# Kernel tuning notes

Hardware: AMD Instinct MI355X
Metric: run time of the kernel (lower is better)

Reference implementation:

```python
import jax, jax.numpy as jnp
import numpy as np

N = 8192
F_IN = 128
F_OUT = 128
NEG_SLOPE = 0.2


def setup_inputs() -> dict:
    key = jax.random.key(0)
    k_h, k_adj, k_W, k_a = jax.random.split(key, 4)
    h = jax.random.normal(k_h, (N, F_IN), dtype=jnp.float32)
    # binary adjacency mask as float (the module multiplies scores by adj)
    adj = (jax.random.uniform(k_adj, (N, N)) < 0.05).astype(jnp.float32)
    # nn.Linear(in, out, bias=False): weight shape [out, in]
    W = jax.random.normal(k_W, (F_OUT, F_IN), dtype=jnp.float32) / np.sqrt(F_IN)
    # nn.Linear(2*out, 1, bias=False): weight shape [1, 2*out]
    a = jax.random.normal(k_a, (1, 2 * F_OUT), dtype=jnp.float32) / np.sqrt(2 * F_OUT)
    return {"h": h, "adj": adj, "W": W, "a": a}


def reference(h, adj, W, a):
    # Wh: [N, F_out]
    Wh = h @ W.T
    f = Wh.shape[-1]
    # a([Wh_i ; Wh_j]) factored: e[i, j] = leaky_relu(Wh[i]@a1 + Wh[j]@a2)
    a1 = a[0, :f]  # [F_out]
    a2 = a[0, f:]  # [F_out]
    s_i = Wh @ a1  # [N]
    s_j = Wh @ a2  # [N]
    e = jax.nn.leaky_relu(s_i[:, None] + s_j[None, :], NEG_SLOPE)  # [N, N]
    # faithful to original: softmax over dim=1 of e * adj (multiplicative mask)
    attention = jax.nn.softmax(e * adj, axis=1)  # [N, N]
    return attention @ Wh  # [N, F_out]
```

## Files before the change

kernel.cpp:

```cpp
#include <hip/hip_runtime.h>

#define N_NODES 8192
#define FDIM 128
#define NEG_SLOPE 0.2f

typedef short short8 __attribute__((ext_vector_type(8)));
typedef float floatx16 __attribute__((ext_vector_type(16)));

__device__ inline unsigned fkey(float x) {
  unsigned b = __float_as_uint(x);
  return (b & 0x80000000u) ? ~b : (b | 0x80000000u);
}
__device__ inline float fkey_dec(unsigned kk) {
  unsigned bb = (kk & 0x80000000u) ? (kk ^ 0x80000000u) : ~kk;
  return __uint_as_float(bb);
}
__device__ inline unsigned short bf16_rn(float x) {
  unsigned u = __float_as_uint(x);
  u += 0x7fffu + ((u >> 16) & 1u);
  return (unsigned short)(u >> 16);
}

__global__ __launch_bounds__(256) void wh_fused_kernel(
    const float* __restrict__ h, const float* __restrict__ W,
    const float* __restrict__ a, float* __restrict__ s1g,
    float* __restrict__ Bj, float* __restrict__ Dj,
    unsigned* __restrict__ s2max_key,
    unsigned short* __restrict__ Bfh, unsigned short* __restrict__ Bfl) {
  __shared__ float Wt[FDIM * 129];
  __shared__ float rows[32 * 132];
  const int t = threadIdx.x;
  const int base = blockIdx.x * 32;
  for (int it = 0; it < 64; ++it) {
    int idx = t + 256 * it;
    int o = idx >> 7, k = idx & 127;
    Wt[k * 129 + o] = W[idx];
  }
  for (int it = 0; it < 16; ++it) {
    int idx = t + 256 * it;
    int r = idx >> 7, col = idx & 127;
    rows[r * 132 + col] = h[(size_t)base * FDIM + idx];
  }
  __syncthreads();
  const int c4 = (t & 31) * 4;
  const int g = t >> 5;
  float acc[4][4];
#pragma unroll
  for (int rr = 0; rr < 4; ++rr)
#pragma unroll
    for (int cc = 0; cc < 4; ++cc) acc[rr][cc] = 0.f;
  for (int k = 0; k < FDIM; ++k) {
    float4 wv = *(const float4*)&Wt[k * 129 + c4];
    float rv[4];
#pragma unroll
    for (int rr = 0; rr < 4; ++rr) rv[rr] = rows[(4 * g + rr) * 132 + k];
#pragma unroll
    for (int rr = 0; rr < 4; ++rr) {
      acc[rr][0] += rv[rr] * wv.x;
      acc[rr][1] += rv[rr] * wv.y;
      acc[rr][2] += rv[rr] * wv.z;
      acc[rr][3] += rv[rr] * wv.w;
    }
  }
  {
    float4 a1c = *(const float4*)&a[c4];
    float4 a2c = *(const float4*)&a[FDIM + c4];
    float p1[4], p2[4];
#pragma unroll
    for (int rr = 0; rr < 4; ++rr) {
      p1[rr] = acc[rr][0] * a1c.x + acc[rr][1] * a1c.y +
               acc[rr][2] * a1c.z + acc[rr][3] * a1c.w;
      p2[rr] = acc[rr][0] * a2c.x + acc[rr][1] * a2c.y +
               acc[rr][2] * a2c.z + acc[rr][3] * a2c.w;
    }
#pragma unroll
    for (int rr = 0; rr < 4; ++rr)
      for (int off = 16; off; off >>= 1) {
        p1[rr] += __shfl_down(p1[rr], off, 32);
        p2[rr] += __shfl_down(p2[rr], off, 32);
      }
    if ((t & 31) == 0) {
      unsigned kmax = 0;
#pragma unroll
      for (int rr = 0; rr < 4; ++rr) {
        int r = base + 4 * g + rr;
        s1g[r] = p1[rr];
        Bj[r] = __expf(p2[rr]);
        Dj[r] = __expf(NEG_SLOPE * p2[rr]);
        unsigned kk = fkey(p2[rr]);
        kmax = kk > kmax ? kk : kmax;
      }
      atomicMax(s2max_key, kmax);
    }
  }
  __syncthreads();
  unsigned short* hbuf = (unsigned short*)Wt;
  unsigned short* lbuf = hbuf + 4096;
#pragma unroll
  for (int rr = 0; rr < 4; ++rr)
#pragma unroll
    for (int cc = 0; cc < 4; ++cc) {
      float x = acc[rr][cc];
      unsigned short hb = bf16_rn(x);
      float hf = __uint_as_float(((unsigned)hb) << 16);
      unsigned short lb = bf16_rn(x - hf);
      int lr = 4 * g + rr;
      int n = c4 + cc;
      int idx = (((lr >> 4) * 4 + (n >> 5)) * 64 + ((lr >> 3) & 1) * 32 +
                 (n & 31)) * 8 + (lr & 7);
      hbuf[idx] = hb;
      lbuf[idx] = lb;
    }
  __syncthreads();
  {
    const unsigned* hsrc = (const unsigned*)hbuf;
    const unsigned* lsrc = (const unsigned*)lbuf;
    unsigned* hdst = (unsigned*)(Bfh + (size_t)base * FDIM);
    unsigned* ldst = (unsigned*)(Bfl + (size_t)base * FDIM);
    for (int q = t; q < 2048; q += 256) { hdst[q] = hsrc[q]; ldst[q] = lsrc[q]; }
  }
}

__global__ __launch_bounds__(256) void gat_mfma_kernel(
    const float* __restrict__ adj,
    const unsigned short* __restrict__ Bfh,
    const unsigned short* __restrict__ Bfl,
    const float* __restrict__ s1g, const float* __restrict__ Bj,
    const float* __restrict__ Dj, const unsigned* __restrict__ s2max_key,
    float* __restrict__ num, float* __restrict__ l_ws) {
  __shared__ float cred[4 * 32 * FDIM];
  const int t = threadIdx.x;
  const int lane = t & 63;
  const int wave = t >> 6;
  const int rowgrp = blockIdx.x >> 1;
  const int ksplit = blockIdx.x & 1;
  const int hh = lane >> 5;
  const int m0 = rowgrp * 32 + (lane & 31);
  const int kbase = ksplit * 4096 + wave * 1024;

  const float s1i = s1g[m0];
  float pmv = s1i + fkey_dec(*s2max_key);
  pmv = pmv > 0.f ? pmv : NEG_SLOPE * pmv;
  const float m = fmaxf(pmv, 0.f);
  const float Ai = __expf(s1i - m);
  const float Ci = __expf(NEG_SLOPE * s1i - m);
  const float Ti = __expf(-s1i);
  const float em = __expf(-m);

  const float* adj_lane = adj + (size_t)m0 * N_NODES + hh * 8;
  const float* bj_lane = Bj + hh * 8;
  const float* dj_lane = Dj + hh * 8;
  const short8* BH = (const short8*)Bfh;
  const short8* BL = (const short8*)Bfl;

  floatx16 acc0, acc1, acc2, acc3;
#pragma unroll
  for (int i = 0; i < 16; ++i) { acc0[i] = 0.f; acc1[i] = 0.f; acc2[i] = 0.f; acc3[i] = 0.f; }
  float rsum = 0.f;

#pragma unroll 2
  for (int k = kbase; k < kbase + 1024; k += 16) {
    float4 a0 = *(const float4*)(adj_lane + k);
    float4 a1 = *(const float4*)(adj_lane + k + 4);
    float4 b0 = *(const float4*)(bj_lane + k);
    float4 b1 = *(const float4*)(bj_lane + k + 4);
    float4 d0 = *(const float4*)(dj_lane + k);
    float4 d1 = *(const float4*)(dj_lane + k + 4);
    size_t fb = ((size_t)(k >> 4) * 4) * 64 + lane;
    short8 bh0 = BH[fb],       bl0 = BL[fb];
    short8 bh1 = BH[fb + 64],  bl1 = BL[fb + 64];
    short8 bh2 = BH[fb + 128], bl2 = BL[fb + 128];
    short8 bh3 = BH[fb + 192], bl3 = BL[fb + 192];

    float av[8] = {a0.x, a0.y, a0.z, a0.w, a1.x, a1.y, a1.z, a1.w};
    float bv[8] = {b0.x, b0.y, b0.z, b0.w, b1.x, b1.y, b1.z, b1.w};
    float dv[8] = {d0.x, d0.y, d0.z, d0.w, d1.x, d1.y, d1.z, d1.w};
    float pv[8];
#pragma unroll
    for (int e = 0; e < 8; ++e) {
      bool cpos = bv[e] > Ti;
      float p = (cpos ? Ai : Ci) * (cpos ? bv[e] : dv[e]);
      p = (av[e] != 0.f) ? p : em;
      pv[e] = p;
      rsum += p;
    }
    union { uint4 u; short8 s; } pk;
    pk.u.x = (unsigned)bf16_rn(pv[0]) | ((unsigned)bf16_rn(pv[1]) << 16);
    pk.u.y = (unsigned)bf16_rn(pv[2]) | ((unsigned)bf16_rn(pv[3]) << 16);
    pk.u.z = (unsigned)bf16_rn(pv[4]) | ((unsigned)bf16_rn(pv[5]) << 16);
    pk.u.w = (unsigned)bf16_rn(pv[6]) | ((unsigned)bf16_rn(pv[7]) << 16);
    short8 af = pk.s;

    acc0 = __builtin_amdgcn_mfma_f32_32x32x16_bf16(af, bh0, acc0, 0, 0, 0);
    acc0 = __builtin_amdgcn_mfma_f32_32x32x16_bf16(af, bl0, acc0, 0, 0, 0);
    acc1 = __builtin_amdgcn_mfma_f32_32x32x16_bf16(af, bh1, acc1, 0, 0, 0);
    acc1 = __builtin_amdgcn_mfma_f32_32x32x16_bf16(af, bl1, acc1, 0, 0, 0);
    acc2 = __builtin_amdgcn_mfma_f32_32x32x16_bf16(af, bh2, acc2, 0, 0, 0);
    acc2 = __builtin_amdgcn_mfma_f32_32x32x16_bf16(af, bl2, acc2, 0, 0, 0);
    acc3 = __builtin_amdgcn_mfma_f32_32x32x16_bf16(af, bh3, acc3, 0, 0, 0);
    acc3 = __builtin_amdgcn_mfma_f32_32x32x16_bf16(af, bl3, acc3, 0, 0, 0);
  }

  rsum += __shfl_xor(rsum, 32);
  if (lane < 32) atomicAdd(&l_ws[rowgrp * 32 + lane], rsum);

#pragma unroll
  for (int reg = 0; reg < 16; ++reg) {
    int r = (reg & 3) + 8 * (reg >> 2) + 4 * hh;
    int cbase = (wave * 32 + r) * FDIM + (lane & 31);
    cred[cbase]      = acc0[reg];
    cred[cbase + 32] = acc1[reg];
    cred[cbase + 64] = acc2[reg];
    cred[cbase + 96] = acc3[reg];
  }
  __syncthreads();
#pragma unroll
  for (int q = 0; q < 16; ++q) {
    int idx = q * 256 + t;
    int r = idx >> 7, c = idx & 127;
    float s = cred[r * FDIM + c] + cred[(32 + r) * FDIM + c] +
              cred[(64 + r) * FDIM + c] + cred[(96 + r) * FDIM + c];
    atomicAdd(&num[(size_t)(rowgrp * 32 + r) * FDIM + c], s);
  }
}

__global__ __launch_bounds__(256) void norm_kernel(
    const float* __restrict__ num, const float* __restrict__ l_ws,
    float* __restrict__ out) {
  int idx = blockIdx.x * 256 + threadIdx.x;
  float4 v = ((const float4*)num)[idx];
  float li = l_ws[idx >> 5];
  ((float4*)out)[idx] =
      make_float4(v.x / li, v.y / li, v.z / li, v.w / li);
}

extern "C" void kernel_launch(void* const* d_in, const int* in_sizes, int n_in,
                              void* d_out, int out_size, void* d_ws, size_t ws_size,
                              hipStream_t stream) {
  const float* h   = (const float*)d_in[0];
  const float* adj = (const float*)d_in[1];
  const float* W   = (const float*)d_in[2];
  const float* a   = (const float*)d_in[3];
  float* out = (float*)d_out;
  float* num = (float*)d_ws;
  float* l_ws = num + (size_t)N_NODES * FDIM;
  unsigned* key = (unsigned*)(l_ws + N_NODES);
  float* s1 = (float*)(key + 1);
  float* Bj = s1 + N_NODES;
  float* Dj = Bj + N_NODES;
  unsigned short* Bfh = (unsigned short*)(Dj + N_NODES);
  unsigned short* Bfl = Bfh + (size_t)N_NODES * FDIM;

  hipMemsetAsync(num, 0, ((size_t)N_NODES * FDIM + N_NODES + 1) * sizeof(float),
                 stream);
  hipLaunchKernelGGL(wh_fused_kernel, dim3(N_NODES / 32), dim3(256), 0, stream,
                     h, W, a, s1, Bj, Dj, key, Bfh, Bfl);
  hipLaunchKernelGGL(gat_mfma_kernel, dim3(512), dim3(256), 0, stream,
                     adj, Bfh, Bfl, s1, Bj, Dj, key, num, l_ws);
  hipLaunchKernelGGL(norm_kernel, dim3(N_NODES * FDIM / 4 / 256), dim3(256), 0,
                     stream, num, l_ws, out);
}
```

Before: 481.4 us.

## Compress adjacency to bitmasks in LDS and compute 64-row tiles per block

Each block now handles 64 rows and a quarter of the columns. It first streams its adjacency tile with coalesced loads and packs it into ballot bitmasks in shared memory. The main loop then computes two 32-row MFMA tiles per wave, so each load of the Bf B-fragments and the Bj/Dj values serves twice as many rows, which halves B-operand traffic per output row. Cross-wave reduction now uses LDS atomics into a 64x128 buffer, followed by global atomics. The cost is more registers (occupancy hinted at 2 blocks), a serial bitmask prologue, and more global atomics per block because of the 4-way K split.

```diff
diff --git a/kernel.cpp b/kernel.cpp
--- a/kernel.cpp
+++ b/kernel.cpp
@@ -6,6 +6,7 @@
 
 typedef short short8 __attribute__((ext_vector_type(8)));
 typedef float floatx16 __attribute__((ext_vector_type(16)));
+typedef unsigned long long u64;
 
 __device__ inline unsigned fkey(float x) {
   unsigned b = __float_as_uint(x);
@@ -121,106 +122,165 @@
   }
 }
 
-__global__ __launch_bounds__(256) void gat_mfma_kernel(
+__global__ __launch_bounds__(256, 2) void gat_mfma_kernel(
     const float* __restrict__ adj,
     const unsigned short* __restrict__ Bfh,
     const unsigned short* __restrict__ Bfl,
     const float* __restrict__ s1g, const float* __restrict__ Bj,
     const float* __restrict__ Dj, const unsigned* __restrict__ s2max_key,
     float* __restrict__ num, float* __restrict__ l_ws) {
-  __shared__ float cred[4 * 32 * FDIM];
+  __shared__ u64 bits_l[64 * 34];
+  __shared__ float cred[64 * FDIM];
   const int t = threadIdx.x;
   const int lane = t & 63;
   const int wave = t >> 6;
-  const int rowgrp = blockIdx.x >> 1;
-  const int ksplit = blockIdx.x & 1;
-  const int hh = lane >> 5;
-  const int m0 = rowgrp * 32 + (lane & 31);
-  const int kbase = ksplit * 4096 + wave * 1024;
-
-  const float s1i = s1g[m0];
-  float pmv = s1i + fkey_dec(*s2max_key);
-  pmv = pmv > 0.f ? pmv : NEG_SLOPE * pmv;
-  const float m = fmaxf(pmv, 0.f);
-  const float Ai = __expf(s1i - m);
-  const float Ci = __expf(NEG_SLOPE * s1i - m);
-  const float Ti = __expf(-s1i);
-  const float em = __expf(-m);
-
-  const float* adj_lane = adj + (size_t)m0 * N_NODES + hh * 8;
-  const float* bj_lane = Bj + hh * 8;
-  const float* dj_lane = Dj + hh * 8;
+  const int rowgrp = blockIdx.x >> 2;
+  const int ksplit = blockIdx.x & 3;
+  const int grow0 = rowgrp * 64;
+  const int blockK0 = ksplit * 2048;
+
+  {
+    const int rb = wave * 16;
+    for (int rl = 0; rl < 16; ++rl) {
+      const int r = rb + rl;
+      const float4* src =
+          (const float4*)(adj + (size_t)(grow0 + r) * N_NODES + blockK0);
+      float4 va[8];
+#pragma unroll
+      for (int sg = 0; sg < 8; ++sg) va[sg] = src[sg * 64 + lane];
+#pragma unroll
+      for (int sg = 0; sg < 8; ++sg) {
+        u64 b0 = __ballot(va[sg].x != 0.f);
+        u64 b1 = __ballot(va[sg].y != 0.f);
+        u64 b2 = __ballot(va[sg].z != 0.f);
+        u64 b3 = __ballot(va[sg].w != 0.f);
+        if (lane < 2) {
+          u64 lo = lane ? b2 : b0;
+          u64 hi = lane ? b3 : b1;
+          u64* dst = &bits_l[r * 34 + sg * 4 + lane * 2];
+          dst[0] = lo;
+          dst[1] = hi;
+        }
+      }
+    }
+  }
+  for (int q = t; q < 64 * FDIM; q += 256) cred[q] = 0.f;
+  __syncthreads();
+
+  const int lq = lane & 31, hh = lane >> 5;
+  const int gr0 = grow0 + lq, gr1 = gr0 + 32;
+  const float s2m = fkey_dec(*s2max_key);
+  const float s10 = s1g[gr0], s11 = s1g[gr1];
+  float pm0 = s10 + s2m; pm0 = pm0 > 0.f ? pm0 : NEG_SLOPE * pm0;
+  float pm1 = s11 + s2m; pm1 = pm1 > 0.f ? pm1 : NEG_SLOPE * pm1;
+  const float m0 = fmaxf(pm0, 0.f), m1 = fmaxf(pm1, 0.f);
+  const float em0 = __expf(-m0), em1 = __expf(-m1);
+  const float Ai0 = __expf(s10 - m0), Ai1 = __expf(s11 - m1);
+  const float Ci0 = __expf(NEG_SLOPE * s10 - m0), Ci1 = __expf(NEG_SLOPE * s11 - m1);
+  const float Ti0 = __expf(-s10), Ti1 = __expf(-s11);
+
   const short8* BH = (const short8*)Bfh;
   const short8* BL = (const short8*)Bfl;
-
-  floatx16 acc0, acc1, acc2, acc3;
-#pragma unroll
-  for (int i = 0; i < 16; ++i) { acc0[i] = 0.f; acc1[i] = 0.f; acc2[i] = 0.f; acc3[i] = 0.f; }
-  float rsum = 0.f;
-
+  floatx16 acc[2][4];
+#pragma unroll
+  for (int mt = 0; mt < 2; ++mt)
+#pragma unroll
+    for (int nt = 0; nt < 4; ++nt)
+#pragma unroll
+      for (int i = 0; i < 16; ++i) acc[mt][nt][i] = 0.f;
+  float rsum0 = 0.f, rsum1 = 0.f;
+
+  for (int s = 0; s < 2; ++s) {
+    const int sg = wave * 2 + s;
+    const u64* bp0 = &bits_l[lq * 34 + sg * 4];
+    const u64* bp1 = &bits_l[(lq + 32) * 34 + sg * 4];
+    longlong2 t0 = *(const longlong2*)bp0;
+    longlong2 t1 = *(const longlong2*)(bp0 + 2);
+    longlong2 t2 = *(const longlong2*)bp1;
+    longlong2 t3 = *(const longlong2*)(bp1 + 2);
+    u64 w0[4] = {(u64)t0.x, (u64)t0.y, (u64)t1.x, (u64)t1.y};
+    u64 w1[4] = {(u64)t2.x, (u64)t2.y, (u64)t3.x, (u64)t3.y};
 #pragma unroll 2
-  for (int k = kbase; k < kbase + 1024; k += 16) {
-    float4 a0 = *(const float4*)(adj_lane + k);
-    float4 a1 = *(const float4*)(adj_lane + k + 4);
-    float4 b0 = *(const float4*)(bj_lane + k);
-    float4 b1 = *(const float4*)(bj_lane + k + 4);
-    float4 d0 = *(const float4*)(dj_lane + k);
-    float4 d1 = *(const float4*)(dj_lane + k + 4);
-    size_t fb = ((size_t)(k >> 4) * 4) * 64 + lane;
-    short8 bh0 = BH[fb],       bl0 = BL[fb];
-    short8 bh1 = BH[fb + 64],  bl1 = BL[fb + 64];
-    short8 bh2 = BH[fb + 128], bl2 = BL[fb + 128];
-    short8 bh3 = BH[fb + 192], bl3 = BL[fb + 192];
-
-    float av[8] = {a0.x, a0.y, a0.z, a0.w, a1.x, a1.y, a1.z, a1.w};
-    float bv[8] = {b0.x, b0.y, b0.z, b0.w, b1.x, b1.y, b1.z, b1.w};
-    float dv[8] = {d0.x, d0.y, d0.z, d0.w, d1.x, d1.y, d1.z, d1.w};
-    float pv[8];
-#pragma unroll
-    for (int e = 0; e < 8; ++e) {
-      bool cpos = bv[e] > Ti;
-      float p = (cpos ? Ai : Ci) * (cpos ? bv[e] : dv[e]);
-      p = (av[e] != 0.f) ? p : em;
-      pv[e] = p;
-      rsum += p;
-    }
-    union { uint4 u; short8 s; } pk;
-    pk.u.x = (unsigned)bf16_rn(pv[0]) | ((unsigned)bf16_rn(pv[1]) << 16);
-    pk.u.y = (unsigned)bf16_rn(pv[2]) | ((unsigned)bf16_rn(pv[3]) << 16);
-    pk.u.z = (unsigned)bf16_rn(pv[4]) | ((unsigned)bf16_rn(pv[5]) << 16);
-    pk.u.w = (unsigned)bf16_rn(pv[6]) | ((unsigned)bf16_rn(pv[7]) << 16);
-    short8 af = pk.s;
-
-    acc0 = __builtin_amdgcn_mfma_f32_32x32x16_bf16(af, bh0, acc0, 0, 0, 0);
-    acc0 = __builtin_amdgcn_mfma_f32_32x32x16_bf16(af, bl0, acc0, 0, 0, 0);
-    acc1 = __builtin_amdgcn_mfma_f32_32x32x16_bf16(af, bh1, acc1, 0, 0, 0);
-    acc1 = __builtin_amdgcn_mfma_f32_32x32x16_bf16(af, bl1, acc1, 0, 0, 0);
-    acc2 = __builtin_amdgcn_mfma_f32_32x32x16_bf16(af, bh2, acc2, 0, 0, 0);
-    acc2 = __builtin_amdgcn_mfma_f32_32x32x16_bf16(af, bl2, acc2, 0, 0, 0);
-    acc3 = __builtin_amdgcn_mfma_f32_32x32x16_bf16(af, bh3, acc3, 0, 0, 0);
-    acc3 = __builtin_amdgcn_mfma_f32_32x32x16_bf16(af, bl3, acc3, 0, 0, 0);
-  }
-
-  rsum += __shfl_xor(rsum, 32);
-  if (lane < 32) atomicAdd(&l_ws[rowgrp * 32 + lane], rsum);
+    for (int it = 0; it < 16; ++it) {
+      const int kg = blockK0 + sg * 256 + it * 16;
+      const int j8 = kg + hh * 8;
+      float4 b0 = *(const float4*)(Bj + j8);
+      float4 b1 = *(const float4*)(Bj + j8 + 4);
+      float4 d0 = *(const float4*)(Dj + j8);
+      float4 d1 = *(const float4*)(Dj + j8 + 4);
+      size_t fb = ((size_t)(kg >> 4)) * 256 + lane;
+      short8 xh0 = BH[fb],       xl0 = BL[fb];
+      short8 xh1 = BH[fb + 64],  xl1 = BL[fb + 64];
+      short8 xh2 = BH[fb + 128], xl2 = BL[fb + 128];
+      short8 xh3 = BH[fb + 192], xl3 = BL[fb + 192];
+      float bvv[8] = {b0.x, b0.y, b0.z, b0.w, b1.x, b1.y, b1.z, b1.w};
+      float dvv[8] = {d0.x, d0.y, d0.z, d0.w, d1.x, d1.y, d1.z, d1.w};
+      const int bsh = it * 4 + hh * 2;
+      float pv0[8], pv1[8];
+#pragma unroll
+      for (int e = 0; e < 8; ++e) {
+        const int sh = bsh + (e >> 2);
+        float f0 = (float)((unsigned)(w0[e & 3] >> sh) & 1u);
+        float f1 = (float)((unsigned)(w1[e & 3] >> sh) & 1u);
+        bool cp0 = bvv[e] > Ti0, cp1 = bvv[e] > Ti1;
+        float q0 = (cp0 ? Ai0 : Ci0) * (cp0 ? bvv[e] : dvv[e]);
+        float q1 = (cp1 ? Ai1 : Ci1) * (cp1 ? bvv[e] : dvv[e]);
+        float p0 = em0 + f0 * (q0 - em0);
+        float p1 = em1 + f1 * (q1 - em1);
+        rsum0 += p0; rsum1 += p1;
+        pv0[e] = p0; pv1[e] = p1;
+      }
+      union { uint4 u; short8 s8; } k0, k1;
+      k0.u.x = (unsigned)bf16_rn(pv0[0]) | ((unsigned)bf16_rn(pv0[1]) << 16);
+      k0.u.y = (unsigned)bf16_rn(pv0[2]) | ((unsigned)bf16_rn(pv0[3]) << 16);
+      k0.u.z = (unsigned)bf16_rn(pv0[4]) | ((unsigned)bf16_rn(pv0[5]) << 16);
+      k0.u.w = (unsigned)bf16_rn(pv0[6]) | ((unsigned)bf16_rn(pv0[7]) << 16);
+      k1.u.x = (unsigned)bf16_rn(pv1[0]) | ((unsigned)bf16_rn(pv1[1]) << 16);
+      k1.u.y = (unsigned)bf16_rn(pv1[2]) | ((unsigned)bf16_rn(pv1[3]) << 16);
+      k1.u.z = (unsigned)bf16_rn(pv1[4]) | ((unsigned)bf16_rn(pv1[5]) << 16);
+      k1.u.w = (unsigned)bf16_rn(pv1[6]) | ((unsigned)bf16_rn(pv1[7]) << 16);
+      short8 af0 = k0.s8, af1 = k1.s8;
+      acc[0][0] = __builtin_amdgcn_mfma_f32_32x32x16_bf16(af0, xh0, acc[0][0], 0, 0, 0);
+      acc[0][0] = __builtin_amdgcn_mfma_f32_32x32x16_bf16(af0, xl0, acc[0][0], 0, 0, 0);
+      acc[0][1] = __builtin_amdgcn_mfma_f32_32x32x16_bf16(af0, xh1, acc[0][1], 0, 0, 0);
+      acc[0][1] = __builtin_amdgcn_mfma_f32_32x32x16_bf16(af0, xl1, acc[0][1], 0, 0, 0);
+      acc[0][2] = __builtin_amdgcn_mfma_f32_32x32x16_bf16(af0, xh2, acc[0][2], 0, 0, 0);
+      acc[0][2] = __builtin_amdgcn_mfma_f32_32x32x16_bf16(af0, xl2, acc[0][2], 0, 0, 0);
+      acc[0][3] = __builtin_amdgcn_mfma_f32_32x32x16_bf16(af0, xh3, acc[0][3], 0, 0, 0);
+      acc[0][3] = __builtin_amdgcn_mfma_f32_32x32x16_bf16(af0, xl3, acc[0][3], 0, 0, 0);
+      acc[1][0] = __builtin_amdgcn_mfma_f32_32x32x16_bf16(af1, xh0, acc[1][0], 0, 0, 0);
+      acc[1][0] = __builtin_amdgcn_mfma_f32_32x32x16_bf16(af1, xl0, acc[1][0], 0, 0, 0);
+      acc[1][1] = __builtin_amdgcn_mfma_f32_32x32x16_bf16(af1, xh1, acc[1][1], 0, 0, 0);
+      acc[1][1] = __builtin_amdgcn_mfma_f32_32x32x16_bf16(af1, xl1, acc[1][1], 0, 0, 0);
+      acc[1][2] = __builtin_amdgcn_mfma_f32_32x32x16_bf16(af1, xh2, acc[1][2], 0, 0, 0);
+      acc[1][2] = __builtin_amdgcn_mfma_f32_32x32x16_bf16(af1, xl2, acc[1][2], 0, 0, 0);
+      acc[1][3] = __builtin_amdgcn_mfma_f32_32x32x16_bf16(af1, xh3, acc[1][3], 0, 0, 0);
+      acc[1][3] = __builtin_amdgcn_mfma_f32_32x32x16_bf16(af1, xl3, acc[1][3], 0, 0, 0);
+    }
+  }
+
+  rsum0 += __shfl_xor(rsum0, 32);
+  rsum1 += __shfl_xor(rsum1, 32);
+  if (lane < 32) {
+    atomicAdd(&l_ws[gr0], rsum0);
+    atomicAdd(&l_ws[gr1], rsum1);
+  }
 
 #pragma unroll
   for (int reg = 0; reg < 16; ++reg) {
-    int r = (reg & 3) + 8 * (reg >> 2) + 4 * hh;
-    int cbase = (wave * 32 + r) * FDIM + (lane & 31);
-    cred[cbase]      = acc0[reg];
-    cred[cbase + 32] = acc1[reg];
-    cred[cbase + 64] = acc2[reg];
-    cred[cbase + 96] = acc3[reg];
-  }
-  __syncthreads();
-#pragma unroll
-  for (int q = 0; q < 16; ++q) {
-    int idx = q * 256 + t;
-    int r = idx >> 7, c = idx & 127;
-    float s = cred[r * FDIM + c] + cred[(32 + r) * FDIM + c] +
-              cred[(64 + r) * FDIM + c] + cred[(96 + r) * FDIM + c];
-    atomicAdd(&num[(size_t)(rowgrp * 32 + r) * FDIM + c], s);
+    const int r = (reg & 3) + 8 * (reg >> 2) + 4 * hh;
+#pragma unroll
+    for (int nt = 0; nt < 4; ++nt) {
+      atomicAdd(&cred[r * FDIM + nt * 32 + lq], acc[0][nt][reg]);
+      atomicAdd(&cred[(r + 32) * FDIM + nt * 32 + lq], acc[1][nt][reg]);
+    }
+  }
+  __syncthreads();
+#pragma unroll
+  for (int q = 0; q < 32; ++q) {
+    const int idx = q * 256 + t;
+    atomicAdd(&num[(size_t)(grow0 + (idx >> 7)) * FDIM + (idx & 127)],
+              cred[idx]);
   }
 }
 
@@ -230,8 +290,7 @@
   int idx = blockIdx.x * 256 + threadIdx.x;
   float4 v = ((const float4*)num)[idx];
   float li = l_ws[idx >> 5];
-  ((float4*)out)[idx] =
-      make_float4(v.x / li, v.y / li, v.z / li, v.w / li);
+  ((float4*)out)[idx] = make_float4(v.x / li, v.y / li, v.z / li, v.w / li);
 }
 
 extern "C" void kernel_launch(void* const* d_in, const int* in_sizes, int n_in,
```

Result: slower. 539.9 us (+12.1%).

## Factor out masked-entry constant, drop bf16 low split, pack adjacency as ballot bitmasks

Applied to the files above, without the earlier changes.

Masked entries all carry the same value exp(-m), so their contribution is handled analytically: the kernel accumulates (p - em) only on nonzero adj entries, and the norm pass adds em times a column sum S of Wh plus N*em to the denominator. The bf16 hi/lo split of Wh is dropped, which halves the B-operand loads and MFMA count but lowers precision. Adjacency is read with coalesced row-wise float4 loads, turned into ballot bitmasks in LDS, and the K range is split four ways across 1024 blocks. Partial results are reduced with LDS atomics into a single 32x128 buffer before the global atomics.

```diff
diff --git a/kernel.cpp b/kernel.cpp
--- a/kernel.cpp
+++ b/kernel.cpp
@@ -6,16 +6,17 @@
 
 typedef short short8 __attribute__((ext_vector_type(8)));
 typedef float floatx16 __attribute__((ext_vector_type(16)));
-
-__device__ inline unsigned fkey(float x) {
+typedef unsigned long long u64;
+
+static __device__ inline unsigned fkey(float x) {
   unsigned b = __float_as_uint(x);
   return (b & 0x80000000u) ? ~b : (b | 0x80000000u);
 }
-__device__ inline float fkey_dec(unsigned kk) {
+static __device__ inline float fkey_dec(unsigned kk) {
   unsigned bb = (kk & 0x80000000u) ? (kk ^ 0x80000000u) : ~kk;
   return __uint_as_float(bb);
 }
-__device__ inline unsigned short bf16_rn(float x) {
+static __device__ inline unsigned short bf16_rn(float x) {
   unsigned u = __float_as_uint(x);
   u += 0x7fffu + ((u >> 16) & 1u);
   return (unsigned short)(u >> 16);
@@ -24,9 +25,8 @@
 __global__ __launch_bounds__(256) void wh_fused_kernel(
     const float* __restrict__ h, const float* __restrict__ W,
     const float* __restrict__ a, float* __restrict__ s1g,
-    float* __restrict__ Bj, float* __restrict__ Dj,
-    unsigned* __restrict__ s2max_key,
-    unsigned short* __restrict__ Bfh, unsigned short* __restrict__ Bfl) {
+    float* __restrict__ Bj, float* __restrict__ Dj, float* __restrict__ S,
+    unsigned* __restrict__ s2max_key, unsigned short* __restrict__ WHf) {
   __shared__ float Wt[FDIM * 129];
   __shared__ float rows[32 * 132];
   const int t = threadIdx.x;
@@ -95,143 +95,170 @@
   }
   __syncthreads();
   unsigned short* hbuf = (unsigned short*)Wt;
-  unsigned short* lbuf = hbuf + 4096;
 #pragma unroll
   for (int rr = 0; rr < 4; ++rr)
 #pragma unroll
     for (int cc = 0; cc < 4; ++cc) {
-      float x = acc[rr][cc];
-      unsigned short hb = bf16_rn(x);
-      float hf = __uint_as_float(((unsigned)hb) << 16);
-      unsigned short lb = bf16_rn(x - hf);
       int lr = 4 * g + rr;
       int n = c4 + cc;
       int idx = (((lr >> 4) * 4 + (n >> 5)) * 64 + ((lr >> 3) & 1) * 32 +
                  (n & 31)) * 8 + (lr & 7);
-      hbuf[idx] = hb;
-      lbuf[idx] = lb;
-    }
+      hbuf[idx] = bf16_rn(acc[rr][cc]);
+    }
+  float4 cs = make_float4(acc[0][0] + acc[1][0] + acc[2][0] + acc[3][0],
+                          acc[0][1] + acc[1][1] + acc[2][1] + acc[3][1],
+                          acc[0][2] + acc[1][2] + acc[2][2] + acc[3][2],
+                          acc[0][3] + acc[1][3] + acc[2][3] + acc[3][3]);
+  *(float4*)&rows[g * FDIM + c4] = cs;
   __syncthreads();
   {
     const unsigned* hsrc = (const unsigned*)hbuf;
-    const unsigned* lsrc = (const unsigned*)lbuf;
-    unsigned* hdst = (unsigned*)(Bfh + (size_t)base * FDIM);
-    unsigned* ldst = (unsigned*)(Bfl + (size_t)base * FDIM);
-    for (int q = t; q < 2048; q += 256) { hdst[q] = hsrc[q]; ldst[q] = lsrc[q]; }
+    unsigned* hdst = (unsigned*)(WHf + (size_t)base * FDIM);
+    for (int q = t; q < 2048; q += 256) hdst[q] = hsrc[q];
+  }
+  if (t < FDIM) {
+    float s = 0.f;
+#pragma unroll
+    for (int gg = 0; gg < 8; ++gg) s += rows[gg * FDIM + t];
+    atomicAdd(&S[t], s);
   }
 }
 
 __global__ __launch_bounds__(256) void gat_mfma_kernel(
-    const float* __restrict__ adj,
-    const unsigned short* __restrict__ Bfh,
-    const unsigned short* __restrict__ Bfl,
+    const float* __restrict__ adj, const unsigned short* __restrict__ WHf,
     const float* __restrict__ s1g, const float* __restrict__ Bj,
     const float* __restrict__ Dj, const unsigned* __restrict__ s2max_key,
     float* __restrict__ num, float* __restrict__ l_ws) {
-  __shared__ float cred[4 * 32 * FDIM];
+  __shared__ u64 bits[4][32][4];
+  __shared__ float cred[32 * FDIM];
   const int t = threadIdx.x;
   const int lane = t & 63;
   const int wave = t >> 6;
-  const int rowgrp = blockIdx.x >> 1;
-  const int ksplit = blockIdx.x & 1;
-  const int hh = lane >> 5;
-  const int m0 = rowgrp * 32 + (lane & 31);
-  const int kbase = ksplit * 4096 + wave * 1024;
-
-  const float s1i = s1g[m0];
-  float pmv = s1i + fkey_dec(*s2max_key);
-  pmv = pmv > 0.f ? pmv : NEG_SLOPE * pmv;
-  const float m = fmaxf(pmv, 0.f);
-  const float Ai = __expf(s1i - m);
-  const float Ci = __expf(NEG_SLOPE * s1i - m);
-  const float Ti = __expf(-s1i);
-  const float em = __expf(-m);
-
-  const float* adj_lane = adj + (size_t)m0 * N_NODES + hh * 8;
-  const float* bj_lane = Bj + hh * 8;
-  const float* dj_lane = Dj + hh * 8;
-  const short8* BH = (const short8*)Bfh;
-  const short8* BL = (const short8*)Bfl;
-
-  floatx16 acc0, acc1, acc2, acc3;
-#pragma unroll
-  for (int i = 0; i < 16; ++i) { acc0[i] = 0.f; acc1[i] = 0.f; acc2[i] = 0.f; acc3[i] = 0.f; }
-  float rsum = 0.f;
-
+  const int lq = lane & 31, hh = lane >> 5;
+  const int rowgrp = blockIdx.x >> 2;
+  const int ksplit = blockIdx.x & 3;
+  const int grow = rowgrp * 32;
+  const int kw0 = ksplit * 2048 + wave * 512;
+
+  for (int q = t; q < 32 * FDIM; q += 256) cred[q] = 0.f;
+  __syncthreads();
+
+  const float s2m = fkey_dec(*s2max_key);
+  const float s1r = s1g[grow + lq];
+  float pm = s1r + s2m;
+  pm = pm > 0.f ? pm : NEG_SLOPE * pm;
+  const float mr = fmaxf(pm, 0.f);
+  const float emr = __expf(-mr);
+  const float Ar = __expf(s1r - mr);
+  const float Cr = __expf(NEG_SLOPE * s1r - mr);
+  const float Tr = __expf(-s1r);
+
+  const short8* BW = (const short8*)WHf;
+  floatx16 acc[4];
+#pragma unroll
+  for (int nt = 0; nt < 4; ++nt)
+#pragma unroll
+    for (int i = 0; i < 16; ++i) acc[nt][i] = 0.f;
+  float lv = 0.f;
+  u64* mybits = &bits[wave][0][0];
+
+  for (int s = 0; s < 2; ++s) {
+    const int c0 = kw0 + s * 256;
+    const float4* ap = (const float4*)(adj + (size_t)grow * N_NODES + c0);
 #pragma unroll 2
-  for (int k = kbase; k < kbase + 1024; k += 16) {
-    float4 a0 = *(const float4*)(adj_lane + k);
-    float4 a1 = *(const float4*)(adj_lane + k + 4);
-    float4 b0 = *(const float4*)(bj_lane + k);
-    float4 b1 = *(const float4*)(bj_lane + k + 4);
-    float4 d0 = *(const float4*)(dj_lane + k);
-    float4 d1 = *(const float4*)(dj_lane + k + 4);
-    size_t fb = ((size_t)(k >> 4) * 4) * 64 + lane;
-    short8 bh0 = BH[fb],       bl0 = BL[fb];
-    short8 bh1 = BH[fb + 64],  bl1 = BL[fb + 64];
-    short8 bh2 = BH[fb + 128], bl2 = BL[fb + 128];
-    short8 bh3 = BH[fb + 192], bl3 = BL[fb + 192];
-
-    float av[8] = {a0.x, a0.y, a0.z, a0.w, a1.x, a1.y, a1.z, a1.w};
-    float bv[8] = {b0.x, b0.y, b0.z, b0.w, b1.x, b1.y, b1.z, b1.w};
-    float dv[8] = {d0.x, d0.y, d0.z, d0.w, d1.x, d1.y, d1.z, d1.w};
-    float pv[8];
-#pragma unroll
-    for (int e = 0; e < 8; ++e) {
-      bool cpos = bv[e] > Ti;
-      float p = (cpos ? Ai : Ci) * (cpos ? bv[e] : dv[e]);
-      p = (av[e] != 0.f) ? p : em;
-      pv[e] = p;
-      rsum += p;
-    }
-    union { uint4 u; short8 s; } pk;
-    pk.u.x = (unsigned)bf16_rn(pv[0]) | ((unsigned)bf16_rn(pv[1]) << 16);
-    pk.u.y = (unsigned)bf16_rn(pv[2]) | ((unsigned)bf16_rn(pv[3]) << 16);
-    pk.u.z = (unsigned)bf16_rn(pv[4]) | ((unsigned)bf16_rn(pv[5]) << 16);
-    pk.u.w = (unsigned)bf16_rn(pv[6]) | ((unsigned)bf16_rn(pv[7]) << 16);
-    short8 af = pk.s;
-
-    acc0 = __builtin_amdgcn_mfma_f32_32x32x16_bf16(af, bh0, acc0, 0, 0, 0);
-    acc0 = __builtin_amdgcn_mfma_f32_32x32x16_bf16(af, bl0, acc0, 0, 0, 0);
-    acc1 = __builtin_amdgcn_mfma_f32_32x32x16_bf16(af, bh1, acc1, 0, 0, 0);
-    acc1 = __builtin_amdgcn_mfma_f32_32x32x16_bf16(af, bl1, acc1, 0, 0, 0);
-    acc2 = __builtin_amdgcn_mfma_f32_32x32x16_bf16(af, bh2, acc2, 0, 0, 0);
-    acc2 = __builtin_amdgcn_mfma_f32_32x32x16_bf16(af, bl2, acc2, 0, 0, 0);
-    acc3 = __builtin_amdgcn_mfma_f32_32x32x16_bf16(af, bh3, acc3, 0, 0, 0);
-    acc3 = __builtin_amdgcn_mfma_f32_32x32x16_bf16(af, bl3, acc3, 0, 0, 0);
-  }
-
-  rsum += __shfl_xor(rsum, 32);
-  if (lane < 32) atomicAdd(&l_ws[rowgrp * 32 + lane], rsum);
-
+    for (int rb = 0; rb < 32; rb += 8) {
+      float4 va[8];
+#pragma unroll
+      for (int r = 0; r < 8; ++r)
+        va[r] = ap[(size_t)(rb + r) * (N_NODES / 4) + lane];
+#pragma unroll
+      for (int r = 0; r < 8; ++r) {
+        u64 b0 = __ballot(va[r].x != 0.f);
+        u64 b1 = __ballot(va[r].y != 0.f);
+        u64 b2 = __ballot(va[r].z != 0.f);
+        u64 b3 = __ballot(va[r].w != 0.f);
+        if (lane == 0) {
+          u64* d = &mybits[(rb + r) * 4];
+          d[0] = b0; d[1] = b1; d[2] = b2; d[3] = b3;
+        }
+      }
+    }
+    ulonglong2 q0 = *(const ulonglong2*)&mybits[lq * 4];
+    ulonglong2 q1 = *(const ulonglong2*)&mybits[lq * 4 + 2];
+    const u64 ws0 = q0.x, ws1 = q0.y, ws2 = q1.x, ws3 = q1.y;
+#pragma unroll 2
+    for (int it = 0; it < 16; ++it) {
+      const int kg = c0 + it * 16;
+      const int j8 = kg + hh * 8;
+      float4 b0 = *(const float4*)(Bj + j8);
+      float4 b1 = *(const float4*)(Bj + j8 + 4);
+      float4 d0 = *(const float4*)(Dj + j8);
+      float4 d1 = *(const float4*)(Dj + j8 + 4);
+      size_t fb = (size_t)(kg >> 4) * 256 + lane;
+      short8 x0 = BW[fb];
+      short8 x1 = BW[fb + 64];
+      short8 x2 = BW[fb + 128];
+      short8 x3 = BW[fb + 192];
+      float bvv[8] = {b0.x, b0.y, b0.z, b0.w, b1.x, b1.y, b1.z, b1.w};
+      float dvv[8] = {d0.x, d0.y, d0.z, d0.w, d1.x, d1.y, d1.z, d1.w};
+      const u64 wsel[4] = {ws0, ws1, ws2, ws3};
+      const int bsh = it * 4 + hh * 2;
+      float vv[8];
+#pragma unroll
+      for (int e = 0; e < 8; ++e) {
+        unsigned bit = (unsigned)(wsel[e & 3] >> (bsh + (e >> 2))) & 1u;
+        bool cp = bvv[e] > Tr;
+        float q = (cp ? Ar : Cr) * (cp ? bvv[e] : dvv[e]);
+        float v = bit ? (q - emr) : 0.f;
+        vv[e] = v;
+        lv += v;
+      }
+      union { uint4 u; short8 s8; } pk;
+      pk.u.x = (unsigned)bf16_rn(vv[0]) | ((unsigned)bf16_rn(vv[1]) << 16);
+      pk.u.y = (unsigned)bf16_rn(vv[2]) | ((unsigned)bf16_rn(vv[3]) << 16);
+      pk.u.z = (unsigned)bf16_rn(vv[4]) | ((unsigned)bf16_rn(vv[5]) << 16);
+      pk.u.w = (unsigned)bf16_rn(vv[6]) | ((unsigned)bf16_rn(vv[7]) << 16);
+      short8 af = pk.s8;
+      acc[0] = __builtin_amdgcn_mfma_f32_32x32x16_bf16(af, x0, acc[0], 0, 0, 0);
+      acc[1] = __builtin_amdgcn_mfma_f32_32x32x16_bf16(af, x1, acc[1], 0, 0, 0);
+      acc[2] = __builtin_amdgcn_mfma_f32_32x32x16_bf16(af, x2, acc[2], 0, 0, 0);
+      acc[3] = __builtin_amdgcn_mfma_f32_32x32x16_bf16(af, x3, acc[3], 0, 0, 0);
+    }
+  }
+  float lvt = lv + __shfl_xor(lv, 32);
+  if (lane < 32) atomicAdd(&l_ws[grow + lq], lvt);
 #pragma unroll
   for (int reg = 0; reg < 16; ++reg) {
-    int r = (reg & 3) + 8 * (reg >> 2) + 4 * hh;
-    int cbase = (wave * 32 + r) * FDIM + (lane & 31);
-    cred[cbase]      = acc0[reg];
-    cred[cbase + 32] = acc1[reg];
-    cred[cbase + 64] = acc2[reg];
-    cred[cbase + 96] = acc3[reg];
-  }
-  __syncthreads();
-#pragma unroll
-  for (int q = 0; q < 16; ++q) {
-    int idx = q * 256 + t;
-    int r = idx >> 7, c = idx & 127;
-    float s = cred[r * FDIM + c] + cred[(32 + r) * FDIM + c] +
-              cred[(64 + r) * FDIM + c] + cred[(96 + r) * FDIM + c];
-    atomicAdd(&num[(size_t)(rowgrp * 32 + r) * FDIM + c], s);
-  }
+    const int r = (reg & 3) + 8 * (reg >> 2) + 4 * hh;
+#pragma unroll
+    for (int nt = 0; nt < 4; ++nt)
+      atomicAdd(&cred[r * FDIM + nt * 32 + lq], acc[nt][reg]);
+  }
+  __syncthreads();
+  for (int q = t; q < 32 * FDIM; q += 256)
+    atomicAdd(&num[(size_t)(grow + (q >> 7)) * FDIM + (q & 127)], cred[q]);
 }
 
 __global__ __launch_bounds__(256) void norm_kernel(
     const float* __restrict__ num, const float* __restrict__ l_ws,
-    float* __restrict__ out) {
-  int idx = blockIdx.x * 256 + threadIdx.x;
-  float4 v = ((const float4*)num)[idx];
-  float li = l_ws[idx >> 5];
-  ((float4*)out)[idx] =
-      make_float4(v.x / li, v.y / li, v.z / li, v.w / li);
+    const float* __restrict__ s1g, const unsigned* __restrict__ s2max_key,
+    const float* __restrict__ S, float* __restrict__ out) {
+  const int idx = blockIdx.x * 256 + threadIdx.x;
+  const int row = idx >> 5;
+  const float s2m = fkey_dec(*s2max_key);
+  float s1r = s1g[row];
+  float pm = s1r + s2m;
+  pm = pm > 0.f ? pm : NEG_SLOPE * pm;
+  float mr = fmaxf(pm, 0.f);
+  float em = __expf(-mr);
+  float l = (float)N_NODES * em + l_ws[row];
+  float inv = 1.f / l;
+  float4 nv = ((const float4*)num)[idx];
+  float4 Sv = ((const float4*)S)[idx & 31];
+  ((float4*)out)[idx] = make_float4((nv.x + em * Sv.x) * inv,
+                                    (nv.y + em * Sv.y) * inv,
+                                    (nv.z + em * Sv.z) * inv,
+                                    (nv.w + em * Sv.w) * inv);
 }
 
 extern "C" void kernel_launch(void* const* d_in, const int* in_sizes, int n_in,
@@ -244,19 +271,20 @@
   float* out = (float*)d_out;
   float* num = (float*)d_ws;
   float* l_ws = num + (size_t)N_NODES * FDIM;
-  unsigned* key = (unsigned*)(l_ws + N_NODES);
-  float* s1 = (float*)(key + 1);
+  float* S = l_ws + N_NODES;
+  unsigned* key = (unsigned*)(S + FDIM);
+  float* s1 = (float*)(key + 4);
   float* Bj = s1 + N_NODES;
   float* Dj = Bj + N_NODES;
-  unsigned short* Bfh = (unsigned short*)(Dj + N_NODES);
-  unsigned short* Bfl = Bfh + (size_t)N_NODES * FDIM;
-
-  hipMemsetAsync(num, 0, ((size_t)N_NODES * FDIM + N_NODES + 1) * sizeof(float),
+  unsigned short* WHf = (unsigned short*)(Dj + N_NODES);
+
+  hipMemsetAsync(num, 0,
+                 ((size_t)N_NODES * FDIM + N_NODES + FDIM + 4) * sizeof(float),
                  stream);
   hipLaunchKernelGGL(wh_fused_kernel, dim3(N_NODES / 32), dim3(256), 0, stream,
-                     h, W, a, s1, Bj, Dj, key, Bfh, Bfl);
-  hipLaunchKernelGGL(gat_mfma_kernel, dim3(512), dim3(256), 0, stream,
-                     adj, Bfh, Bfl, s1, Bj, Dj, key, num, l_ws);
+                     h, W, a, s1, Bj, Dj, S, key, WHf);
+  hipLaunchKernelGGL(gat_mfma_kernel, dim3(1024), dim3(256), 0, stream,
+                     adj, WHf, s1, Bj, Dj, key, num, l_ws);
   hipLaunchKernelGGL(norm_kernel, dim3(N_NODES * FDIM / 4 / 256), dim3(256), 0,
-                     stream, num, l_ws, out);
-}
+                     stream, num, l_ws, s1, key, S, out);
+}
```

Result: no change. 490.2 us (+1.8%).
